# Performance work log

Measured on AMD Instinct MI355X. Metric: run time of the kernel, lower is better.

## Reference

```python
import jax, jax.numpy as jnp
import numpy as np

N_NODES = 100000
N_EDGES = 1600000
N_REL = 8
IN_CH = 64
HIDDEN = 64
OUT_CH = 32


def setup_inputs() -> dict:
    key = jax.random.key(0)
    ks = jax.random.split(key, 10)
    s_in = 1.0 / np.sqrt(IN_CH)
    s_h = 1.0 / np.sqrt(HIDDEN)
    return {
        "x": jax.random.normal(ks[0], (N_NODES, IN_CH), dtype=jnp.float32),
        "edge_index": jax.random.randint(ks[1], (2, N_EDGES), 0, N_NODES, dtype=jnp.int64),
        "edge_type": jax.random.randint(ks[2], (N_EDGES,), 0, N_REL, dtype=jnp.int64),
        "W0": jax.random.normal(ks[3], (N_REL, IN_CH, HIDDEN), dtype=jnp.float32) * s_in,
        "Q0": jax.random.normal(ks[4], (HIDDEN, 1), dtype=jnp.float32) * s_h,
        "K0": jax.random.normal(ks[5], (HIDDEN, 1), dtype=jnp.float32) * s_h,
        "b0": jnp.zeros((HIDDEN,), dtype=jnp.float32),
        "W1": jax.random.normal(ks[6], (N_REL, HIDDEN, OUT_CH), dtype=jnp.float32) * s_h,
        "Q1": jax.random.normal(ks[7], (OUT_CH, 1), dtype=jnp.float32) * (1.0 / np.sqrt(OUT_CH)),
        "K1": jax.random.normal(ks[8], (OUT_CH, 1), dtype=jnp.float32) * (1.0 / np.sqrt(OUT_CH)),
        "b1": jnp.zeros((OUT_CH,), dtype=jnp.float32),
    }


def rgat_conv(x, src, dst, et, W, Q, K, b, n_nodes):
    # relation-typed transform of all nodes: [R, N, out]
    xw = jnp.einsum("ni,rio->rno", x, W)
    # per-node, per-relation attention logits (heads=1, dim=1)
    q = jnp.einsum("rno,od->rnd", xw, Q)[..., 0]  # [R, N]
    k = jnp.einsum("rno,od->rnd", xw, K)[..., 0]  # [R, N]
    # additive self-attention, leaky_relu slope 0.2 (PyG RGATConv default)
    alpha = jax.nn.leaky_relu(q[et, dst] + k[et, src], negative_slope=0.2)  # [E]
    # across-relation segment softmax over incoming edges of each dst node
    amax = jax.ops.segment_max(alpha, dst, num_segments=n_nodes)
    a = jnp.exp(alpha - amax[dst])
    denom = jax.ops.segment_sum(a, dst, num_segments=n_nodes)
    a = a / (denom[dst] + 1e-16)
    # weighted scatter-add aggregation of transformed source features
    msg = a[:, None] * xw[et, src]  # [E, out]
    return jax.ops.segment_sum(msg, dst, num_segments=n_nodes) + b


def reference(x, edge_index, edge_type, W0, Q0, K0, b0, W1, Q1, K1, b1):
    src, dst = edge_index[0], edge_index[1]
    n = x.shape[0]
    h = rgat_conv(x, src, dst, edge_type, W0, Q0, K0, b0, n)
    h = jax.nn.relu(h)  # dropout p=0.0 -> identity
    out = rgat_conv(h, src, dst, edge_type, W1, Q1, K1, b1, n)
    return out
```

## Files before the change

kernel.cpp:

```cpp
#include <hip/hip_runtime.h>
#include <hip/hip_bf16.h>
#include <math.h>


#define CSR_CHUNK 8192

__global__ void k_bhist(const int* __restrict__ dst, int* __restrict__ bcount,
                        int E, int NB) {
    __shared__ int h[512];
    int t = threadIdx.x;
    for (int i = t; i < NB; i += 256) h[i] = 0;
    __syncthreads();
    int e0 = blockIdx.x * CSR_CHUNK;
    int e1 = min(e0 + CSR_CHUNK, E);
    for (int i = e0 + t; i < e1; i += 256) atomicAdd(&h[dst[i] >> 8], 1);
    __syncthreads();
    for (int i = t; i < NB; i += 256) {
        int c = h[i];
        if (c) atomicAdd(&bcount[i], c);
    }
}

__global__ void k_bscan(const int* __restrict__ bcount, int* __restrict__ bstart,
                        int* __restrict__ gcur, int* __restrict__ rowptr,
                        int NB, int N, int E) {
    __shared__ int s[512];
    int t = threadIdx.x;
    int v = (t < NB) ? bcount[t] : 0;
    s[t] = v;
    __syncthreads();
    for (int off = 1; off < 512; off <<= 1) {
        int a = (t >= off) ? s[t - off] : 0;
        __syncthreads();
        s[t] += a;
        __syncthreads();
    }
    int excl = s[t] - v;
    if (t < NB) {
        bstart[t] = excl;
        gcur[t] = excl;
    }
    if (t == 0) {
        bstart[NB] = E;
        rowptr[N] = E;
    }
}

__global__ void k_bscatter(const int* __restrict__ src, const int* __restrict__ dst,
                           const int* __restrict__ et, int* __restrict__ gcur,
                           unsigned* __restrict__ ebuf, int E, int NB) {
    __shared__ int h[512];
    __shared__ int basearr[512];
    int t = threadIdx.x;
    for (int i = t; i < NB; i += 256) h[i] = 0;
    __syncthreads();
    int e0 = blockIdx.x * CSR_CHUNK;
    int e1 = min(e0 + CSR_CHUNK, E);
    for (int i = e0 + t; i < e1; i += 256) atomicAdd(&h[dst[i] >> 8], 1);
    __syncthreads();
    for (int i = t; i < NB; i += 256) {
        int c = h[i];
        basearr[i] = c ? atomicAdd(&gcur[i], c) : 0;
        h[i] = 0;
    }
    __syncthreads();
    for (int i = e0 + t; i < e1; i += 256) {
        int d = dst[i];
        int b = d >> 8;
        int off = atomicAdd(&h[b], 1);
        ebuf[basearr[b] + off] =
            ((unsigned)(d & 255) << 20) | ((unsigned)et[i] << 17) | (unsigned)src[i];
    }
}

__global__ void k_bsort(const unsigned* __restrict__ ebuf, const int* __restrict__ bstart,
                        int* __restrict__ rowptr, int* __restrict__ csr, int N) {
    __shared__ int lh[2048];
    __shared__ int ls[2048];
    __shared__ int ss[256];
    int b = blockIdx.x, t = threadIdx.x;
    int e0 = bstart[b], e1 = bstart[b + 1];
    for (int i = t; i < 2048; i += 256) lh[i] = 0;
    __syncthreads();
    for (int i = e0 + t; i < e1; i += 256) {
        unsigned u = ebuf[i];
        atomicAdd(&lh[(int)(((u >> 20) & 255) * 8 + ((u >> 17) & 7))], 1);
    }
    __syncthreads();
    int loc[8];
    int s = 0;
#pragma unroll
    for (int j = 0; j < 8; j++) {
        loc[j] = s;
        s += lh[t * 8 + j];
    }
    ss[t] = s;
    __syncthreads();
    for (int off = 1; off < 256; off <<= 1) {
        int a = (t >= off) ? ss[t - off] : 0;
        __syncthreads();
        ss[t] += a;
        __syncthreads();
    }
    int excl = ss[t] - s;
#pragma unroll
    for (int j = 0; j < 8; j++) ls[t * 8 + j] = excl + loc[j];
    int node = b * 256 + t;
    if (node < N) rowptr[node] = e0 + excl;
    __syncthreads();
    for (int i = t; i < 2048; i += 256) lh[i] = 0;
    __syncthreads();
    for (int i = e0 + t; i < e1; i += 256) {
        unsigned u = ebuf[i];
        int key = (int)(((u >> 20) & 255) * 8 + ((u >> 17) & 7));
        int off = atomicAdd(&lh[key], 1);
        csr[e0 + ls[key] + off] = (int)(u & 0xFFFFF);
    }
}


__global__ void k_wt2(const float* __restrict__ W, __hip_bfloat16* __restrict__ hi,
                      __hip_bfloat16* __restrict__ lo, int OUT, int total) {
    int t = blockIdx.x * blockDim.x + threadIdx.x;
    if (t < total) {
        int per = 64 * OUT;
        int r = t / per;
        int rem = t % per;
        int i = rem / OUT;
        int o = rem % OUT;
        float v = W[t];
        __hip_bfloat16 h = __float2bfloat16(v);
        __hip_bfloat16 l = __float2bfloat16(v - __bfloat162float(h));
        size_t idx = (size_t)o * 512 + i * 8 + r;
        hi[idx] = h;
        lo[idx] = l;
    }
}

__global__ void k_wqk(const float* W, const float* Qv, const float* Kv,
                      float* wq, float* wk, int OUT) {
    int t = blockIdx.x * blockDim.x + threadIdx.x;
    if (t < 8 * 64) {
        int r = t >> 6, i = t & 63;
        const float* wrow = W + ((size_t)r * 64 + i) * OUT;
        float a = 0.f, b = 0.f;
        for (int o = 0; o < OUT; o++) {
            float w = wrow[o];
            a += w * Qv[o];
            b += w * Kv[o];
        }
        wq[t] = a;
        wk[t] = b;
    }
}

__global__ __launch_bounds__(256) void k_qk2(
        const float* __restrict__ xin, const float* __restrict__ wq,
        const float* __restrict__ wk, float* __restrict__ qn,
        float* __restrict__ kn, unsigned short* __restrict__ xbb, int N) {
    __shared__ float xt[64][65];
    __shared__ float swq[8 * 65], swk[8 * 65];
    int t = threadIdx.x;
    int nb0 = blockIdx.x * 64;
    for (int i = t; i < 512; i += 256) {
        int r = i >> 6, c = i & 63;
        swq[r * 65 + c] = wq[i];
        swk[r * 65 + c] = wk[i];
    }
    for (int i = t; i < 1024; i += 256) {
        int ns = i >> 4;
        int c4 = i & 15;
        int n = nb0 + ns;
        float4 v = {0.f, 0.f, 0.f, 0.f};
        if (n < N) v = ((const float4*)xin)[(size_t)n * 16 + c4];
        xt[ns][c4 * 4 + 0] = v.x;
        xt[ns][c4 * 4 + 1] = v.y;
        xt[ns][c4 * 4 + 2] = v.z;
        xt[ns][c4 * 4 + 3] = v.w;
        if (n < N) {
            __hip_bfloat16 b0 = __float2bfloat16(v.x);
            __hip_bfloat16 b1 = __float2bfloat16(v.y);
            __hip_bfloat16 b2 = __float2bfloat16(v.z);
            __hip_bfloat16 b3 = __float2bfloat16(v.w);
            ushort4 o;
            o.x = *(unsigned short*)&b0;
            o.y = *(unsigned short*)&b1;
            o.z = *(unsigned short*)&b2;
            o.w = *(unsigned short*)&b3;
            *(ushort4*)(xbb + (size_t)n * 64 + c4 * 4) = o;
        }
    }
    __syncthreads();
#pragma unroll
    for (int g = t; g < 512; g += 256) {
        int ns = g >> 3, r = g & 7;
        int n = nb0 + ns;
        if (n < N) {
            float qa = 0.f, ka = 0.f;
#pragma unroll
            for (int i = 0; i < 64; i++) {
                float xv = xt[ns][i];
                qa += xv * swq[r * 65 + i];
                ka += xv * swk[r * 65 + i];
            }
            qn[(size_t)n * 8 + r] = qa;
            kn[(size_t)n * 8 + r] = ka;
        }
    }
}

__global__ __launch_bounds__(256) void k_agg4(
        const int* __restrict__ rowptr, const int* __restrict__ csr,
        const float* __restrict__ qn, const float* __restrict__ kn,
        const unsigned short* __restrict__ xb,
        __hip_bfloat16* __restrict__ z, int N) {
    int wid = (blockIdx.x * blockDim.x + threadIdx.x) >> 6;
    int lane = threadIdx.x & 63;
    if (wid >= N) return;
    int r0 = rowptr[wid], r1 = rowptr[wid + 1];

    float qv = (lane < 8) ? qn[wid * 8 + lane] : 0.f;

    float denom = 0.f;
    float a0 = 0.f, a1 = 0.f, a2 = 0.f, a3 = 0.f;
    float a4 = 0.f, a5 = 0.f, a6 = 0.f, a7 = 0.f;
    int currel = 0;
    float racc = 0.f;

    for (int base = r0; base < r1; base += 64) {
        int s = base + lane;
        int pk = (s < r1) ? csr[s] : 0;
        int src = pk & 0x1FFFF;
        int rel = pk >> 17;
        float q = __shfl(qv, rel, 64);
        float tv = 0.f;
        if (s < r1) {
            float v = q + kn[src * 8 + rel];
            v = (v >= 0.f) ? v : 0.2f * v;
            tv = __expf(v);
        }
        float ts = tv;
#pragma unroll
        for (int off = 32; off > 0; off >>= 1) ts += __shfl_xor(ts, off, 64);
        denom += ts;

        int cnt = min(64, r1 - base);
        int tvi = (int)__float_as_uint(tv);
        for (int j = 0; j < cnt; j += 16) {
            unsigned p[16];
            float t[16];
#pragma unroll
            for (int u = 0; u < 16; u++) {
                p[u] = (unsigned)__builtin_amdgcn_readlane(pk, j + u);
                t[u] = __uint_as_float((unsigned)__builtin_amdgcn_readlane(tvi, j + u));
            }
            unsigned xu[16];
#pragma unroll
            for (int u = 0; u < 16; u++)
                xu[u] = (unsigned)xb[(size_t)(p[u] & 0x1FFFF) * 64 + lane];
#pragma unroll
            for (int u = 0; u < 16; u++) {
                int rl = (int)(p[u] >> 17);
                if (rl != currel) {
                    switch (currel) {
                        case 0: a0 += racc; break;
                        case 1: a1 += racc; break;
                        case 2: a2 += racc; break;
                        case 3: a3 += racc; break;
                        case 4: a4 += racc; break;
                        case 5: a5 += racc; break;
                        case 6: a6 += racc; break;
                        case 7: a7 += racc; break;
                    }
                    currel = rl;
                    racc = 0.f;
                }
                racc += t[u] * __uint_as_float(xu[u] << 16);
            }
        }
    }
    switch (currel) {
        case 0: a0 += racc; break;
        case 1: a1 += racc; break;
        case 2: a2 += racc; break;
        case 3: a3 += racc; break;
        case 4: a4 += racc; break;
        case 5: a5 += racc; break;
        case 6: a6 += racc; break;
        case 7: a7 += racc; break;
    }

    float inv = 1.f / (denom + 1e-16f);
    unsigned short u[8];
    float av[8] = {a0, a1, a2, a3, a4, a5, a6, a7};
#pragma unroll
    for (int r = 0; r < 8; r++) {
        __hip_bfloat16 b = __float2bfloat16(av[r] * inv);
        u[r] = *(unsigned short*)&b;
    }
    uint4 pack;
    pack.x = (unsigned)u[0] | ((unsigned)u[1] << 16);
    pack.y = (unsigned)u[2] | ((unsigned)u[3] << 16);
    pack.z = (unsigned)u[4] | ((unsigned)u[5] << 16);
    pack.w = (unsigned)u[6] | ((unsigned)u[7] << 16);
    *(uint4*)((unsigned short*)z + (size_t)wid * 512 + lane * 8) = pack;
}

template <int OUT, bool RELU>
__global__ __launch_bounds__(256) void k_zw(
        const __hip_bfloat16* __restrict__ z,
        const __hip_bfloat16* __restrict__ wthi, const __hip_bfloat16* __restrict__ wtlo,
        const float* __restrict__ bias, float* __restrict__ xout, int N) {
    using v8s = __attribute__((ext_vector_type(8))) short;
    using v4f = __attribute__((ext_vector_type(4))) float;
    constexpr int NT = OUT / 16;
    int wave = threadIdx.x >> 6;
    int lane = threadIdx.x & 63;
    int quad = lane >> 4;
    int l15 = lane & 15;
    int m0 = (blockIdx.x * 4 + wave) * 32;
    if (m0 >= N) return;

    v4f acc[NT][2];
#pragma unroll
    for (int nt = 0; nt < NT; nt++) {
        acc[nt][0] = (v4f){0.f, 0.f, 0.f, 0.f};
        acc[nt][1] = (v4f){0.f, 0.f, 0.f, 0.f};
    }

    const short* zp = (const short*)z;
    const short* wh = (const short*)wthi;
    const short* wl = (const short*)wtlo;
    int n0 = m0 + l15, n1 = m0 + 16 + l15;

    for (int k0 = 0; k0 < 512; k0 += 32) {
        int koff = k0 + quad * 8;
        v8s A0 = {}, A1 = {};
        if (n0 < N) A0 = *(const v8s*)(zp + (size_t)n0 * 512 + koff);
        if (n1 < N) A1 = *(const v8s*)(zp + (size_t)n1 * 512 + koff);
#pragma unroll
        for (int nt = 0; nt < NT; nt++) {
            v8s bh = *(const v8s*)(wh + (size_t)(nt * 16 + l15) * 512 + koff);
            v8s bl = *(const v8s*)(wl + (size_t)(nt * 16 + l15) * 512 + koff);
            acc[nt][0] = __builtin_amdgcn_mfma_f32_16x16x32_bf16(A0, bh, acc[nt][0], 0, 0, 0);
            acc[nt][0] = __builtin_amdgcn_mfma_f32_16x16x32_bf16(A0, bl, acc[nt][0], 0, 0, 0);
            acc[nt][1] = __builtin_amdgcn_mfma_f32_16x16x32_bf16(A1, bh, acc[nt][1], 0, 0, 0);
            acc[nt][1] = __builtin_amdgcn_mfma_f32_16x16x32_bf16(A1, bl, acc[nt][1], 0, 0, 0);
        }
    }

#pragma unroll
    for (int nt = 0; nt < NT; nt++) {
        float bcol = bias[nt * 16 + l15];
#pragma unroll
        for (int mm = 0; mm < 2; mm++) {
#pragma unroll
            for (int g = 0; g < 4; g++) {
                int row = m0 + mm * 16 + quad * 4 + g;
                if (row < N) {
                    float o = acc[nt][mm][g] + bcol;
                    if (RELU) o = fmaxf(o, 0.f);
                    xout[(size_t)row * OUT + nt * 16 + l15] = o;
                }
            }
        }
    }
}


extern "C" void kernel_launch(void* const* d_in, const int* in_sizes, int n_in,
                              void* d_out, int out_size, void* d_ws, size_t ws_size,
                              hipStream_t stream) {
    const float* x   = (const float*)d_in[0];
    const int*   ei  = (const int*)d_in[1];
    const int*   et  = (const int*)d_in[2];
    const float* W0  = (const float*)d_in[3];
    const float* Q0  = (const float*)d_in[4];
    const float* K0  = (const float*)d_in[5];
    const float* b0  = (const float*)d_in[6];
    const float* W1  = (const float*)d_in[7];
    const float* Q1  = (const float*)d_in[8];
    const float* K1  = (const float*)d_in[9];
    const float* b1  = (const float*)d_in[10];
    float* out = (float*)d_out;

    const int N = in_sizes[0] / 64;
    const int E = in_sizes[2];
    const int* src = ei;
    const int* dst = ei + E;
    const int NB = (N + 255) >> 8;

    char* p = (char*)d_ws;
    auto alloc = [&](size_t bytes) -> void* {
        void* r = (void*)p;
        p += ((bytes + 255) / 256) * 256;
        return r;
    };
    int* rowptr   = (int*)alloc((size_t)(N + 1) * 4);
    int* bcount   = (int*)alloc(513 * 4);
    int* bstart   = (int*)alloc(513 * 4);
    int* gcur     = (int*)alloc(513 * 4);
    unsigned* ebuf = (unsigned*)alloc((size_t)E * 4);
    int* csr      = (int*)alloc((size_t)E * 4);
    float* wq     = (float*)alloc(8 * 64 * 4);
    float* wk     = (float*)alloc(8 * 64 * 4);
    float* qn     = (float*)alloc((size_t)N * 8 * 4);
    float* kn     = (float*)alloc((size_t)N * 8 * 4);
    __hip_bfloat16* wthi = (__hip_bfloat16*)alloc((size_t)64 * 512 * 2);
    __hip_bfloat16* wtlo = (__hip_bfloat16*)alloc((size_t)64 * 512 * 2);
    __hip_bfloat16* z    = (__hip_bfloat16*)alloc((size_t)N * 512 * 2);
    float* h      = (float*)alloc((size_t)N * 64 * 4);
    unsigned short* xbb = (unsigned short*)alloc((size_t)N * 64 * 2);

    int nchunks = (E + CSR_CHUNK - 1) / CSR_CHUNK;
    hipMemsetAsync(bcount, 0, (size_t)NB * 4, stream);
    k_bhist<<<nchunks, 256, 0, stream>>>(dst, bcount, E, NB);
    k_bscan<<<1, 512, 0, stream>>>(bcount, bstart, gcur, rowptr, NB, N, E);
    k_bscatter<<<nchunks, 256, 0, stream>>>(src, dst, et, gcur, ebuf, E, NB);
    k_bsort<<<NB, 256, 0, stream>>>(ebuf, bstart, rowptr, csr, N);

    int naggb = (N * 64 + 255) / 256;
    int nzwb = (N + 127) / 128;
    int nqkb = (N + 63) / 64;

    k_wqk<<<2, 256, 0, stream>>>(W0, Q0, K0, wq, wk, 64);
    k_qk2<<<nqkb, 256, 0, stream>>>(x, wq, wk, qn, kn, xbb, N);
    k_wt2<<<(8 * 64 * 64 + 255) / 256, 256, 0, stream>>>(W0, wthi, wtlo, 64, 8 * 64 * 64);
    k_agg4<<<naggb, 256, 0, stream>>>(rowptr, csr, qn, kn, xbb, z, N);
    k_zw<64, true><<<nzwb, 256, 0, stream>>>(z, wthi, wtlo, b0, h, N);

    k_wqk<<<2, 256, 0, stream>>>(W1, Q1, K1, wq, wk, 32);
    k_qk2<<<nqkb, 256, 0, stream>>>(h, wq, wk, qn, kn, xbb, N);
    k_wt2<<<(8 * 64 * 32 + 255) / 256, 256, 0, stream>>>(W1, wthi, wtlo, 32, 8 * 64 * 32);
    k_agg4<<<naggb, 256, 0, stream>>>(rowptr, csr, qn, kn, xbb, z, N);
    k_zw<32, false><<<nzwb, 256, 0, stream>>>(z, wthi, wtlo, b1, out, N);
}
```

Baseline: 490.0 us.

## Fuse edge aggregation with relation-weight MFMA GEMM via LDS staging

Merges the per-node attention aggregation kernel and the z·W MFMA GEMM into one kernel. Each block aggregates 16 nodes into an LDS tile of bf16 relation-partial sums, then waves run MFMA against the split hi/lo weights and write the output directly. This removes the large global intermediate z buffer and its write and read traffic. In exchange it uses about 16 KB of LDS per block, serializes 4 nodes per wave, and leaves waves idle in the MFMA phase when OUT=32.

```diff
diff --git a/kernel.cpp b/kernel.cpp
--- a/kernel.cpp
+++ b/kernel.cpp
@@ -209,159 +209,139 @@
     }
 }
 
-__global__ __launch_bounds__(256) void k_agg4(
+#define ZSTR 520
+template <int OUT, bool RELU>
+__global__ __launch_bounds__(256) void k_fused(
         const int* __restrict__ rowptr, const int* __restrict__ csr,
         const float* __restrict__ qn, const float* __restrict__ kn,
         const unsigned short* __restrict__ xb,
-        __hip_bfloat16* __restrict__ z, int N) {
-    int wid = (blockIdx.x * blockDim.x + threadIdx.x) >> 6;
-    int lane = threadIdx.x & 63;
-    if (wid >= N) return;
-    int r0 = rowptr[wid], r1 = rowptr[wid + 1];
-
-    float qv = (lane < 8) ? qn[wid * 8 + lane] : 0.f;
-
-    float denom = 0.f;
-    float a0 = 0.f, a1 = 0.f, a2 = 0.f, a3 = 0.f;
-    float a4 = 0.f, a5 = 0.f, a6 = 0.f, a7 = 0.f;
-    int currel = 0;
-    float racc = 0.f;
-
-    for (int base = r0; base < r1; base += 64) {
-        int s = base + lane;
-        int pk = (s < r1) ? csr[s] : 0;
-        int src = pk & 0x1FFFF;
-        int rel = pk >> 17;
-        float q = __shfl(qv, rel, 64);
-        float tv = 0.f;
-        if (s < r1) {
-            float v = q + kn[src * 8 + rel];
-            v = (v >= 0.f) ? v : 0.2f * v;
-            tv = __expf(v);
-        }
-        float ts = tv;
-#pragma unroll
-        for (int off = 32; off > 0; off >>= 1) ts += __shfl_xor(ts, off, 64);
-        denom += ts;
-
-        int cnt = min(64, r1 - base);
-        int tvi = (int)__float_as_uint(tv);
-        for (int j = 0; j < cnt; j += 16) {
-            unsigned p[16];
-            float t[16];
-#pragma unroll
-            for (int u = 0; u < 16; u++) {
-                p[u] = (unsigned)__builtin_amdgcn_readlane(pk, j + u);
-                t[u] = __uint_as_float((unsigned)__builtin_amdgcn_readlane(tvi, j + u));
-            }
-            unsigned xu[16];
-#pragma unroll
-            for (int u = 0; u < 16; u++)
-                xu[u] = (unsigned)xb[(size_t)(p[u] & 0x1FFFF) * 64 + lane];
-#pragma unroll
-            for (int u = 0; u < 16; u++) {
-                int rl = (int)(p[u] >> 17);
-                if (rl != currel) {
-                    switch (currel) {
-                        case 0: a0 += racc; break;
-                        case 1: a1 += racc; break;
-                        case 2: a2 += racc; break;
-                        case 3: a3 += racc; break;
-                        case 4: a4 += racc; break;
-                        case 5: a5 += racc; break;
-                        case 6: a6 += racc; break;
-                        case 7: a7 += racc; break;
-                    }
-                    currel = rl;
-                    racc = 0.f;
-                }
-                racc += t[u] * __uint_as_float(xu[u] << 16);
-            }
-        }
-    }
-    switch (currel) {
-        case 0: a0 += racc; break;
-        case 1: a1 += racc; break;
-        case 2: a2 += racc; break;
-        case 3: a3 += racc; break;
-        case 4: a4 += racc; break;
-        case 5: a5 += racc; break;
-        case 6: a6 += racc; break;
-        case 7: a7 += racc; break;
-    }
-
-    float inv = 1.f / (denom + 1e-16f);
-    unsigned short u[8];
-    float av[8] = {a0, a1, a2, a3, a4, a5, a6, a7};
-#pragma unroll
-    for (int r = 0; r < 8; r++) {
-        __hip_bfloat16 b = __float2bfloat16(av[r] * inv);
-        u[r] = *(unsigned short*)&b;
-    }
-    uint4 pack;
-    pack.x = (unsigned)u[0] | ((unsigned)u[1] << 16);
-    pack.y = (unsigned)u[2] | ((unsigned)u[3] << 16);
-    pack.z = (unsigned)u[4] | ((unsigned)u[5] << 16);
-    pack.w = (unsigned)u[6] | ((unsigned)u[7] << 16);
-    *(uint4*)((unsigned short*)z + (size_t)wid * 512 + lane * 8) = pack;
-}
-
-template <int OUT, bool RELU>
-__global__ __launch_bounds__(256) void k_zw(
-        const __hip_bfloat16* __restrict__ z,
-        const __hip_bfloat16* __restrict__ wthi, const __hip_bfloat16* __restrict__ wtlo,
+        const __hip_bfloat16* __restrict__ wthi,
+        const __hip_bfloat16* __restrict__ wtlo,
         const float* __restrict__ bias, float* __restrict__ xout, int N) {
     using v8s = __attribute__((ext_vector_type(8))) short;
     using v4f = __attribute__((ext_vector_type(4))) float;
-    constexpr int NT = OUT / 16;
-    int wave = threadIdx.x >> 6;
+    __shared__ unsigned short zt[16 * ZSTR];
+    int wv = threadIdx.x >> 6;
     int lane = threadIdx.x & 63;
+    int nb0 = blockIdx.x * 16;
+
+    for (int q = 0; q < 4; q++) {
+        int nl = wv * 4 + q;
+        int wid = nb0 + nl;
+        uint4 pack = {0u, 0u, 0u, 0u};
+        if (wid < N) {
+            int r0 = rowptr[wid], r1 = rowptr[wid + 1];
+            float qv = (lane < 8) ? qn[wid * 8 + lane] : 0.f;
+            float denom = 0.f;
+            float a0 = 0.f, a1 = 0.f, a2 = 0.f, a3 = 0.f;
+            float a4 = 0.f, a5 = 0.f, a6 = 0.f, a7 = 0.f;
+            int currel = 0;
+            float racc = 0.f;
+
+            for (int base = r0; base < r1; base += 64) {
+                int s = base + lane;
+                int pk = (s < r1) ? csr[s] : 0;
+                int src = pk & 0x1FFFF;
+                int rel = pk >> 17;
+                float qq = __shfl(qv, rel, 64);
+                float tv = 0.f;
+                if (s < r1) {
+                    float v = qq + kn[src * 8 + rel];
+                    v = (v >= 0.f) ? v : 0.2f * v;
+                    tv = __expf(v);
+                }
+                float ts = tv;
+#pragma unroll
+                for (int off = 32; off > 0; off >>= 1) ts += __shfl_xor(ts, off, 64);
+                denom += ts;
+
+                int cnt = min(64, r1 - base);
+                int tvi = (int)__float_as_uint(tv);
+                for (int j = 0; j < cnt; j += 16) {
+                    unsigned p[16];
+                    float t[16];
+#pragma unroll
+                    for (int u = 0; u < 16; u++) {
+                        p[u] = (unsigned)__builtin_amdgcn_readlane(pk, j + u);
+                        t[u] = __uint_as_float(
+                            (unsigned)__builtin_amdgcn_readlane(tvi, j + u));
+                    }
+                    unsigned xu[16];
+#pragma unroll
+                    for (int u = 0; u < 16; u++)
+                        xu[u] = (unsigned)xb[(size_t)(p[u] & 0x1FFFF) * 64 + lane];
+#pragma unroll
+                    for (int u = 0; u < 16; u++) {
+                        int rl = (int)(p[u] >> 17);
+                        if (rl != currel) {
+                            switch (currel) {
+                                case 0: a0 += racc; break;
+                                case 1: a1 += racc; break;
+                                case 2: a2 += racc; break;
+                                case 3: a3 += racc; break;
+                                case 4: a4 += racc; break;
+                                case 5: a5 += racc; break;
+                                case 6: a6 += racc; break;
+                                case 7: a7 += racc; break;
+                            }
+                            currel = rl;
+                            racc = 0.f;
+                        }
+                        racc += t[u] * __uint_as_float(xu[u] << 16);
+                    }
+                }
+            }
+            switch (currel) {
+                case 0: a0 += racc; break;
+                case 1: a1 += racc; break;
+                case 2: a2 += racc; break;
+                case 3: a3 += racc; break;
+                case 4: a4 += racc; break;
+                case 5: a5 += racc; break;
+                case 6: a6 += racc; break;
+                case 7: a7 += racc; break;
+            }
+            float inv = 1.f / (denom + 1e-16f);
+            float av[8] = {a0, a1, a2, a3, a4, a5, a6, a7};
+            unsigned short u[8];
+#pragma unroll
+            for (int r = 0; r < 8; r++) {
+                __hip_bfloat16 b = __float2bfloat16(av[r] * inv);
+                u[r] = *(unsigned short*)&b;
+            }
+            pack.x = (unsigned)u[0] | ((unsigned)u[1] << 16);
+            pack.y = (unsigned)u[2] | ((unsigned)u[3] << 16);
+            pack.z = (unsigned)u[4] | ((unsigned)u[5] << 16);
+            pack.w = (unsigned)u[6] | ((unsigned)u[7] << 16);
+        }
+        *(uint4*)&zt[nl * ZSTR + lane * 8] = pack;
+    }
+    __syncthreads();
+
     int quad = lane >> 4;
     int l15 = lane & 15;
-    int m0 = (blockIdx.x * 4 + wave) * 32;
-    if (m0 >= N) return;
-
-    v4f acc[NT][2];
-#pragma unroll
-    for (int nt = 0; nt < NT; nt++) {
-        acc[nt][0] = (v4f){0.f, 0.f, 0.f, 0.f};
-        acc[nt][1] = (v4f){0.f, 0.f, 0.f, 0.f};
-    }
-
-    const short* zp = (const short*)z;
-    const short* wh = (const short*)wthi;
-    const short* wl = (const short*)wtlo;
-    int n0 = m0 + l15, n1 = m0 + 16 + l15;
-
-    for (int k0 = 0; k0 < 512; k0 += 32) {
-        int koff = k0 + quad * 8;
-        v8s A0 = {}, A1 = {};
-        if (n0 < N) A0 = *(const v8s*)(zp + (size_t)n0 * 512 + koff);
-        if (n1 < N) A1 = *(const v8s*)(zp + (size_t)n1 * 512 + koff);
-#pragma unroll
-        for (int nt = 0; nt < NT; nt++) {
+    int nt = wv;
+    if (nt * 16 < OUT) {
+        const short* wh = (const short*)wthi;
+        const short* wl = (const short*)wtlo;
+        v4f acc = {0.f, 0.f, 0.f, 0.f};
+#pragma unroll
+        for (int k0 = 0; k0 < 512; k0 += 32) {
+            int koff = k0 + quad * 8;
+            v8s A = *(const v8s*)&zt[l15 * ZSTR + koff];
             v8s bh = *(const v8s*)(wh + (size_t)(nt * 16 + l15) * 512 + koff);
             v8s bl = *(const v8s*)(wl + (size_t)(nt * 16 + l15) * 512 + koff);
-            acc[nt][0] = __builtin_amdgcn_mfma_f32_16x16x32_bf16(A0, bh, acc[nt][0], 0, 0, 0);
-            acc[nt][0] = __builtin_amdgcn_mfma_f32_16x16x32_bf16(A0, bl, acc[nt][0], 0, 0, 0);
-            acc[nt][1] = __builtin_amdgcn_mfma_f32_16x16x32_bf16(A1, bh, acc[nt][1], 0, 0, 0);
-            acc[nt][1] = __builtin_amdgcn_mfma_f32_16x16x32_bf16(A1, bl, acc[nt][1], 0, 0, 0);
-        }
-    }
-
-#pragma unroll
-    for (int nt = 0; nt < NT; nt++) {
+            acc = __builtin_amdgcn_mfma_f32_16x16x32_bf16(A, bh, acc, 0, 0, 0);
+            acc = __builtin_amdgcn_mfma_f32_16x16x32_bf16(A, bl, acc, 0, 0, 0);
+        }
         float bcol = bias[nt * 16 + l15];
 #pragma unroll
-        for (int mm = 0; mm < 2; mm++) {
-#pragma unroll
-            for (int g = 0; g < 4; g++) {
-                int row = m0 + mm * 16 + quad * 4 + g;
-                if (row < N) {
-                    float o = acc[nt][mm][g] + bcol;
-                    if (RELU) o = fmaxf(o, 0.f);
-                    xout[(size_t)row * OUT + nt * 16 + l15] = o;
-                }
+        for (int g = 0; g < 4; g++) {
+            int row = nb0 + quad * 4 + g;
+            if (row < N) {
+                float o = acc[g] + bcol;
+                if (RELU) o = fmaxf(o, 0.f);
+                xout[(size_t)row * OUT + nt * 16 + l15] = o;
             }
         }
     }
@@ -408,7 +388,6 @@
     float* kn     = (float*)alloc((size_t)N * 8 * 4);
     __hip_bfloat16* wthi = (__hip_bfloat16*)alloc((size_t)64 * 512 * 2);
     __hip_bfloat16* wtlo = (__hip_bfloat16*)alloc((size_t)64 * 512 * 2);
-    __hip_bfloat16* z    = (__hip_bfloat16*)alloc((size_t)N * 512 * 2);
     float* h      = (float*)alloc((size_t)N * 64 * 4);
     unsigned short* xbb = (unsigned short*)alloc((size_t)N * 64 * 2);
 
@@ -419,19 +398,18 @@
     k_bscatter<<<nchunks, 256, 0, stream>>>(src, dst, et, gcur, ebuf, E, NB);
     k_bsort<<<NB, 256, 0, stream>>>(ebuf, bstart, rowptr, csr, N);
 
-    int naggb = (N * 64 + 255) / 256;
-    int nzwb = (N + 127) / 128;
+    int nfb = (N + 15) / 16;
     int nqkb = (N + 63) / 64;
 
     k_wqk<<<2, 256, 0, stream>>>(W0, Q0, K0, wq, wk, 64);
     k_qk2<<<nqkb, 256, 0, stream>>>(x, wq, wk, qn, kn, xbb, N);
     k_wt2<<<(8 * 64 * 64 + 255) / 256, 256, 0, stream>>>(W0, wthi, wtlo, 64, 8 * 64 * 64);
-    k_agg4<<<naggb, 256, 0, stream>>>(rowptr, csr, qn, kn, xbb, z, N);
-    k_zw<64, true><<<nzwb, 256, 0, stream>>>(z, wthi, wtlo, b0, h, N);
+    k_fused<64, true><<<nfb, 256, 0, stream>>>(rowptr, csr, qn, kn, xbb,
+                                               wthi, wtlo, b0, h, N);
 
     k_wqk<<<2, 256, 0, stream>>>(W1, Q1, K1, wq, wk, 32);
     k_qk2<<<nqkb, 256, 0, stream>>>(h, wq, wk, qn, kn, xbb, N);
     k_wt2<<<(8 * 64 * 32 + 255) / 256, 256, 0, stream>>>(W1, wthi, wtlo, 32, 8 * 64 * 32);
-    k_agg4<<<naggb, 256, 0, stream>>>(rowptr, csr, qn, kn, xbb, z, N);
-    k_zw<32, false><<<nzwb, 256, 0, stream>>>(z, wthi, wtlo, b1, out, N);
-}
+    k_fused<32, false><<<nfb, 256, 0, stream>>>(rowptr, csr, qn, kn, xbb,
+                                                wthi, wtlo, b1, out, N);
+}
```

New measurement: 446.1 us. 9.0% less time.
